# Kernel optimization log

Measured on AMD Instinct MI355X. Metric: run time of the kernel, lower is better.

Reference implementation:

```python
import jax, jax.numpy as jnp
import numpy as np

S, L, E = 64, 256, 768          # sentences, tokens per sentence, BERT hidden
N, P = 4096, 32768              # events, event pairs
C, H, D = 256, 4, 64            # CGE channels, heads, head dim (C = H*D = n_last)
M = 8                           # max event span length
MLP_H = 1024
ITERS = 3                       # max_iteration + 1
RATE = 0.5
BETA_INTRA, BETA_INTER = 0.5, 0.5


def setup_inputs():
    key = jax.random.key(0)
    ks = jax.random.split(key, 16)
    nrm = lambda k, shape, sc: jax.random.normal(k, shape, dtype=jnp.float32) * sc
    event_start = jax.random.randint(ks[2], (N,), 0, L - M)
    span = jax.random.randint(ks[3], (N,), 1, M + 1)
    return {
        "sent_emb": nrm(ks[0], (S, L, E), 1.0),
        "proj_in_W": nrm(ks[7], (E, C), E ** -0.5),
        "proj_in_b": jnp.zeros((C,), jnp.float32),
        "proj_W": nrm(ks[8], (C, C), C ** -0.5),
        "proj_b": jnp.zeros((C,), jnp.float32),
        "att_src_intra": nrm(ks[9], (H, D), D ** -0.5),
        "att_dst_intra": nrm(ks[10], (H, D), D ** -0.5),
        "att_src_inter": nrm(ks[11], (H, D), D ** -0.5),
        "att_dst_inter": nrm(ks[12], (H, D), D ** -0.5),
        "mlp_W1": nrm(ks[13], (C + 2 * E, MLP_H), (C + 2 * E) ** -0.5),
        "mlp_b1": jnp.zeros((MLP_H,), jnp.float32),
        "mlp_W2": nrm(ks[14], (MLP_H, 3), MLP_H ** -0.5),
        "mlp_b2": jnp.zeros((3,), jnp.float32),
        "event_sent": jax.random.randint(ks[1], (N,), 0, S),
        "event_start": event_start,
        "event_end": event_start + span,
        "pair_idx": jax.random.randint(ks[4], (P, 2), 0, N),
        "rel_type": jax.random.randint(ks[5], (P,), 0, 2),
        "target": jax.random.randint(ks[6], (P,), 0, 3),
    }


def _attend(h, src, dst, emask, att_src, att_dst):
    # h: [N,H,D]. Masked graph attention, softmax over incoming edges per dst.
    a = jax.nn.leaky_relu((h[src] * att_src).sum(-1) + (h[dst] * att_dst).sum(-1), 0.2)  # [En,H]
    a = jnp.where(emask[:, None], a, -1e9)
    amax = jnp.maximum(jax.ops.segment_max(a, dst, num_segments=N), -1e9)  # [N,H]
    ex = jnp.exp(a - amax[dst]) * emask[:, None].astype(a.dtype)
    denom = jax.ops.segment_sum(ex, dst, num_segments=N)
    alpha = ex / (denom[dst] + 1e-9)
    out = jax.ops.segment_sum(alpha[:, :, None] * h[src], dst, num_segments=N)  # [N,H,D]
    return out.reshape(N, H * D)


def _forward(sent_emb, proj_in_W, proj_in_b, proj_W, proj_b,
             att_src_intra, att_dst_intra, att_src_inter, att_dst_inter,
             mlp_W1, mlp_b1, mlp_W2, mlp_b2,
             event_sent, event_start, event_end, pair_idx, rel_type, target):
    # extract_event: mean of sentence token embeddings over each event span
    pos = event_start[:, None] + jnp.arange(M)                      # [N,M]
    vmask = (pos < event_end[:, None]).astype(sent_emb.dtype)       # [N,M]
    tok = sent_emb[event_sent[:, None], jnp.clip(pos, 0, L - 1)]    # [N,M,E]
    e_emb = (tok * vmask[..., None]).sum(1) / (event_end - event_start).astype(sent_emb.dtype)[:, None]

    p0, p1 = pair_idx[:, 0], pair_idx[:, 1]
    pair_emb = jnp.concatenate([e_emb[p0], e_emb[p1]], axis=-1)     # [P,2E]
    x = e_emb @ proj_in_W + proj_in_b                               # [N,C]

    self_idx = jnp.arange(N)
    ones_n = jnp.ones((N,), bool)
    src_all = jnp.concatenate([p0, p1])
    dst_all = jnp.concatenate([p1, p0])
    intra2 = jnp.concatenate([rel_type == 0, rel_type == 0])

    loss = jnp.float32(0.0)
    pred = None
    for it in range(ITERS):
        diff = x[p0] - x[p1]                                        # [P,C]
        pre = jnp.concatenate([pair_emb, diff], axis=-1)            # [P,2E+C]
        pred = jax.nn.relu(pre @ mlp_W1 + mlp_b1) @ mlp_W2 + mlp_b2  # [P,3]
        logp = jax.nn.log_softmax(pred, axis=-1)
        loss = loss + (1.0 / (it + 1)) * (-jnp.take_along_axis(logp, target[:, None], axis=1).mean())

        # data-dependent edge construction (masked, fixed-size edge lists)
        psoft = jax.nn.softmax(pred, axis=-1)
        conf = psoft.max(1) > RATE
        parg = psoft.argmax(1)
        m_all = jnp.concatenate([conf & (parg == 1), conf & (parg == 2)])

        h = (x @ proj_W + proj_b).reshape(N, H, D)
        # intra edges + always-on self loops
        src_i = jnp.concatenate([src_all, self_idx])
        dst_i = jnp.concatenate([dst_all, self_idx])
        m_i = jnp.concatenate([m_all & intra2, ones_n])
        out_intra = _attend(h, src_i, dst_i, m_i, att_src_intra, att_dst_intra)
        out_inter = _attend(h, src_all, dst_all, m_all & (~intra2), att_src_inter, att_dst_inter)
        x = BETA_INTRA * out_intra + BETA_INTER * out_inter
    return loss, pred


def reference(sent_emb, proj_in_W, proj_in_b, proj_W, proj_b,
              att_src_intra, att_dst_intra, att_src_inter, att_dst_inter,
              mlp_W1, mlp_b1, mlp_W2, mlp_b2,
              event_sent, event_start, event_end, pair_idx, rel_type, target):
    return _forward(sent_emb, proj_in_W, proj_in_b, proj_W, proj_b,
                    att_src_intra, att_dst_intra, att_src_inter, att_dst_inter,
                    mlp_W1, mlp_b1, mlp_W2, mlp_b2,
                    event_sent, event_start, event_end, pair_idx, rel_type, target)
```

## Files before the change

### kernel.cpp

```cpp
#include <hip/hip_runtime.h>
#include <cstddef>
#include <cstdint>

#define NEV   4096
#define NPAIR 32768
#define NEDGE (2*NPAIR)
#define EDIM  768
#define CDIM  256
#define MLPH  1024
#define LLEN  256

typedef unsigned short u16;
typedef __attribute__((ext_vector_type(8))) short bhalf8;
typedef __attribute__((ext_vector_type(4))) float f32x4;

#define GLOAD_LDS(g, l) __builtin_amdgcn_global_load_lds( \
    (const __attribute__((address_space(1))) unsigned int*)(g), \
    (__attribute__((address_space(3))) unsigned int*)(l), 16, 0, 0)

__device__ inline u16 f2bf(float f) {
  union { float f; unsigned u; } v; v.f = f;
  unsigned r = v.u + 0x7fffu + ((v.u >> 16) & 1u);
  return (u16)(r >> 16);
}
__device__ inline float bf2f(u16 h) {
  union { unsigned u; float f; } v; v.u = ((unsigned)h) << 16; return v.f;
}

__global__ void k_zero(int* __restrict__ deg, float* __restrict__ out) {
  int i = blockIdx.x * 256 + threadIdx.x;
  if (i < NEV) deg[i] = 0;
  if (i == 0) out[0] = 0.f;
}

__global__ void k_embed(const float* __restrict__ sent, const int* __restrict__ es,
                        const int* __restrict__ st, const int* __restrict__ en,
                        u16* __restrict__ Ahat) {
  int node = blockIdx.x;
  int s = es[node];
  int a = st[node];
  int span = en[node] - a;
  float fspan = (float)span;
  const float* base = sent + ((size_t)s * LLEN + a) * EDIM;
  for (int d = threadIdx.x; d < EDIM; d += 256) {
    float acc = 0.f;
    for (int m = 0; m < span; ++m) acc += base[(size_t)m * EDIM + d];
    float e = acc / fspan;
    u16 hi = f2bf(e);
    float lo = e - bf2f(hi);
    size_t b = (size_t)node * (3 * EDIM);
    Ahat[b + d] = hi;
    Ahat[b + EDIM + d] = hi;
    Ahat[b + 2 * EDIM + d] = f2bf(lo);
  }
}

__global__ void k_count(const int* __restrict__ pair, int* __restrict__ deg) {
  int e = blockIdx.x * 256 + threadIdx.x;
  if (e >= NEDGE) return;
  int p = (e < NPAIR) ? e : e - NPAIR;
  int dst = (e < NPAIR) ? pair[2 * p + 1] : pair[2 * p];
  atomicAdd(&deg[dst], 1);
}

__global__ void k_scan(const int* __restrict__ deg, int* __restrict__ rowp,
                       int* __restrict__ cursor) {
  __shared__ int part[256];
  int t = threadIdx.x;
  int base = t * 16;
  int sum = 0;
  for (int i = 0; i < 16; ++i) sum += deg[base + i];
  part[t] = sum;
  __syncthreads();
  for (int off = 1; off < 256; off <<= 1) {
    int v = (t >= off) ? part[t - off] : 0;
    __syncthreads();
    part[t] += v;
    __syncthreads();
  }
  int run = (t == 0) ? 0 : part[t - 1];
  for (int i = 0; i < 16; ++i) {
    rowp[base + i] = run;
    cursor[base + i] = 0;
    run += deg[base + i];
  }
  if (t == 255) rowp[NEV] = run;
}

__global__ void k_scatter(const int* __restrict__ pair, const int* __restrict__ rowp,
                          int* __restrict__ cursor, int* __restrict__ e_src,
                          int* __restrict__ e_id) {
  int e = blockIdx.x * 256 + threadIdx.x;
  if (e >= NEDGE) return;
  int p   = (e < NPAIR) ? e : e - NPAIR;
  int src = (e < NPAIR) ? pair[2 * p]     : pair[2 * p + 1];
  int dst = (e < NPAIR) ? pair[2 * p + 1] : pair[2 * p];
  int pos = rowp[dst] + atomicAdd(&cursor[dst], 1);
  e_src[pos] = src;
  e_id[pos]  = e;
}

__global__ __launch_bounds__(256) void cvt_w(const float* __restrict__ W1,
                                             const float* __restrict__ piW,
                                             const float* __restrict__ projW,
                                             u16* __restrict__ BT, int which)
{
  __shared__ float tile[32][33];
  int K = which ? CDIM : EDIM;
  int ld = K * 3;
  int bk = blockIdx.y * 32;
  int bc = blockIdx.x * 32;
  int tx = threadIdx.x & 31, ty = threadIdx.x >> 5;
#pragma unroll
  for (int rr = 0; rr < 4; ++rr) {
    int k = bk + ty + rr * 8;
    int c = bc + tx;
    float v;
    if (which == 0) {
      v = (c < 1024) ? W1[(size_t)k * MLPH + c]
        : (c < 2048) ? W1[(size_t)(EDIM + k) * MLPH + (c - 1024)]
        : piW[(size_t)k * CDIM + (c - 2048)];
    } else {
      v = (c < 1024) ? W1[(size_t)(2 * EDIM + k) * MLPH + c]
        : projW[(size_t)k * CDIM + (c - 1024)];
    }
    tile[ty + rr * 8][tx] = v;
  }
  __syncthreads();
#pragma unroll
  for (int rr = 0; rr < 4; ++rr) {
    int c = bc + ty + rr * 8;
    int k = bk + tx;
    float v = tile[tx][ty + rr * 8];
    u16 hi = f2bf(v);
    float lo = v - bf2f(hi);
    size_t b = (size_t)c * ld;
    BT[b + k] = hi;
    BT[b + K + k] = f2bf(lo);
    BT[b + 2 * K + k] = hi;
  }
}

__global__ __launch_bounds__(256) void mgemm(
    const u16* __restrict__ A, const u16* __restrict__ BT, int Kp, int mode,
    float* __restrict__ G1, float* __restrict__ G2, u16* __restrict__ Xhat,
    const float* __restrict__ pib, const float* __restrict__ b1,
    const float* __restrict__ pb, float* __restrict__ U, float* __restrict__ V,
    float* __restrict__ h)
{
  __shared__ u16 As[64 * 64];
  __shared__ u16 Bs[128 * 64];
  int tid = threadIdx.x;
  int wave = tid >> 6, lane = tid & 63;
  int bm = blockIdx.y * 64, bn = blockIdx.x * 128;
  int wm = (wave >> 1) * 32, wn = (wave & 1) * 64;

  int srow = tid >> 3;
  int scol = (tid & 7) << 3;
  const u16* Ag = A + (size_t)(bm + srow) * Kp + scol;
  const u16* Bg = BT + (size_t)(bn + srow) * Kp + scol;
  u16* Asd = &As[tid * 8];
  u16* Bsd = &Bs[tid * 8];

  f32x4 acc[2][4];
#pragma unroll
  for (int i = 0; i < 2; ++i)
#pragma unroll
    for (int j = 0; j < 4; ++j) {
      f32x4 z = {0.f, 0.f, 0.f, 0.f};
      acc[i][j] = z;
    }

  int fr = lane & 15;
  int fq = lane >> 4;

  for (int k0 = 0; k0 < Kp; k0 += 64) {
#pragma unroll
    for (int c = 0; c < 2; ++c)
      GLOAD_LDS(Ag + (size_t)(c * 32) * Kp, Asd + c * 2048);
#pragma unroll
    for (int c = 0; c < 4; ++c)
      GLOAD_LDS(Bg + (size_t)(c * 32) * Kp, Bsd + c * 2048);
    __syncthreads();
#pragma unroll
    for (int kk = 0; kk < 2; ++kk) {
      bhalf8 af[2], bf[4];
#pragma unroll
      for (int i = 0; i < 2; ++i)
        af[i] = *(const bhalf8*)&As[(wm + i * 16 + fr) * 64 + kk * 32 + fq * 8];
#pragma unroll
      for (int j = 0; j < 4; ++j)
        bf[j] = *(const bhalf8*)&Bs[(wn + j * 16 + fr) * 64 + kk * 32 + fq * 8];
#pragma unroll
      for (int i = 0; i < 2; ++i)
#pragma unroll
        for (int j = 0; j < 4; ++j)
          acc[i][j] = __builtin_amdgcn_mfma_f32_16x16x32_bf16(af[i], bf[j], acc[i][j], 0, 0, 0);
    }
    __syncthreads();
    Ag += 64;
    Bg += 64;
  }

#pragma unroll
  for (int i = 0; i < 2; ++i) {
    int mrow = bm + wm + i * 16 + fq * 4;
#pragma unroll
    for (int g = 0; g < 4; ++g) {
      int m = mrow + g;
#pragma unroll
      for (int j = 0; j < 4; ++j) {
        int c = bn + wn + j * 16 + fr;
        float vv = acc[i][j][g];
        if (mode == 0) {
          if (c < 1024) {
            G1[(size_t)m * MLPH + c] = vv;
          } else if (c < 2048) {
            G2[(size_t)m * MLPH + (c - 1024)] = vv;
          } else {
            int cc = c - 2048;
            float xv = vv + pib[cc];
            u16 hi = f2bf(xv);
            float lo = xv - bf2f(hi);
            size_t b = (size_t)m * (3 * CDIM);
            Xhat[b + cc] = hi;
            Xhat[b + CDIM + cc] = hi;
            Xhat[b + 2 * CDIM + cc] = f2bf(lo);
          }
        } else {
          if (c < 1024) {
            size_t idx = (size_t)m * MLPH + c;
            U[idx] = G1[idx] + vv + b1[c];
            V[idx] = G2[idx] - vv;
          } else {
            int cc = c - 1024;
            h[(size_t)m * CDIM + cc] = vv + pb[cc];
          }
        }
      }
    }
  }
}

__global__ void k_s(const float* __restrict__ h,
                    const float* __restrict__ asi, const float* __restrict__ adi,
                    const float* __restrict__ asj, const float* __restrict__ adj,
                    float* __restrict__ sv) {
  int node = blockIdx.x * 4 + (threadIdx.x >> 6);
  int lane = threadIdx.x & 63;
  int head = lane >> 4;
  int d0 = (lane & 15) << 2;
  float4 hv = *(const float4*)(h + (size_t)node * CDIM + head * 64 + d0);
  float4 w1 = *(const float4*)(asi + head * 64 + d0);
  float4 w2 = *(const float4*)(adi + head * 64 + d0);
  float4 w3 = *(const float4*)(asj + head * 64 + d0);
  float4 w4 = *(const float4*)(adj + head * 64 + d0);
  float p1 = hv.x * w1.x + hv.y * w1.y + hv.z * w1.z + hv.w * w1.w;
  float p2 = hv.x * w2.x + hv.y * w2.y + hv.z * w2.z + hv.w * w2.w;
  float p3 = hv.x * w3.x + hv.y * w3.y + hv.z * w3.z + hv.w * w3.w;
  float p4 = hv.x * w4.x + hv.y * w4.y + hv.z * w4.z + hv.w * w4.w;
#pragma unroll
  for (int m = 1; m < 16; m <<= 1) {
    p1 += __shfl_xor(p1, m);
    p2 += __shfl_xor(p2, m);
    p3 += __shfl_xor(p3, m);
    p4 += __shfl_xor(p4, m);
  }
  if ((lane & 15) == 0) {
    sv[0 * NEV * 4 + node * 4 + head] = p1;
    sv[1 * NEV * 4 + node * 4 + head] = p2;
    sv[2 * NEV * 4 + node * 4 + head] = p3;
    sv[3 * NEV * 4 + node * 4 + head] = p4;
  }
}

__global__ __launch_bounds__(256) void k_pred(
    const float* __restrict__ U, const float* __restrict__ V,
    const int* __restrict__ pair, const float* __restrict__ W2,
    const float* __restrict__ b2, const int* __restrict__ target,
    int* __restrict__ mstate, float* __restrict__ out,
    float* __restrict__ partials, float lossCoef)
{
  __shared__ float red[4];
  int wv = threadIdx.x >> 6;
  int p = blockIdx.x * 4 + wv;
  int lane = threadIdx.x & 63;
  int i0 = pair[2 * p], i1 = pair[2 * p + 1];
  const float* u = U + (size_t)i0 * MLPH;
  const float* v = V + (size_t)i1 * MLPH;
  float a0 = 0.f, a1 = 0.f, a2 = 0.f;
  for (int kb = (lane << 2); kb < MLPH; kb += 256) {
    float4 uu = *(const float4*)(u + kb);
    float4 vv = *(const float4*)(v + kb);
    float h0 = fmaxf(uu.x + vv.x, 0.f);
    float h1 = fmaxf(uu.y + vv.y, 0.f);
    float h2 = fmaxf(uu.z + vv.z, 0.f);
    float h3 = fmaxf(uu.w + vv.w, 0.f);
    const float4* w4 = (const float4*)(W2 + 3 * kb);
    float4 wa = w4[0], wb = w4[1], wc = w4[2];
    a0 += h0 * wa.x + h1 * wa.w + h2 * wb.z + h3 * wc.y;
    a1 += h0 * wa.y + h1 * wb.x + h2 * wb.w + h3 * wc.z;
    a2 += h0 * wa.z + h1 * wb.y + h2 * wc.x + h3 * wc.w;
  }
#pragma unroll
  for (int m = 32; m >= 1; m >>= 1) {
    a0 += __shfl_down(a0, m);
    a1 += __shfl_down(a1, m);
    a2 += __shfl_down(a2, m);
  }
  if (lane == 0) {
    a0 += b2[0]; a1 += b2[1]; a2 += b2[2];
    float mx = fmaxf(a0, fmaxf(a1, a2));
    float e0 = expf(a0 - mx), e1 = expf(a1 - mx), e2 = expf(a2 - mx);
    float sum = e0 + e1 + e2;
    int arg = 0; float best = e0;
    if (e1 > best) { best = e1; arg = 1; }
    if (e2 > best) { best = e2; arg = 2; }
    bool conf = (best / sum) > 0.5f;
    mstate[p] = conf ? arg : -1;
    int t = target[p];
    float predt = (t == 0) ? a0 : ((t == 1) ? a1 : a2);
    float logp = (predt - mx) - logf(sum);
    red[wv] = -logp * lossCoef;
    float* po = out + 1 + (size_t)p * 3;
    po[0] = a0; po[1] = a1; po[2] = a2;
  }
  __syncthreads();
  if (threadIdx.x == 0) partials[blockIdx.x] = red[0] + red[1] + red[2] + red[3];
}

__global__ void k_lossred(const float* __restrict__ partials, float* __restrict__ out, int n) {
  __shared__ float sm[256];
  float s = 0.f;
  for (int i = threadIdx.x; i < n; i += 256) s += partials[i];
  sm[threadIdx.x] = s;
  __syncthreads();
  for (int off = 128; off; off >>= 1) {
    if (threadIdx.x < off) sm[threadIdx.x] += sm[threadIdx.x + off];
    __syncthreads();
  }
  if (threadIdx.x == 0) out[0] += sm[0];
}

__global__ __launch_bounds__(256) void k_attn(
    const float* __restrict__ h, const float* __restrict__ sv,
    const int* __restrict__ rowp, const int* __restrict__ e_src,
    const int* __restrict__ e_id, const int* __restrict__ mstate,
    const int* __restrict__ rel, u16* __restrict__ Xhat)
{
  int node = blockIdx.x;
  int t = threadIdx.x;
  int head = t >> 6;
  const float* s_si = sv;
  const float* s_di = sv + NEV * 4;
  const float* s_sj = sv + 2 * NEV * 4;
  const float* s_dj = sv + 3 * NEV * 4;
  float sdi = s_di[node * 4 + head];
  float sdj = s_dj[node * 4 + head];
  int beg = rowp[node], end = rowp[node + 1];
  float aself = s_si[node * 4 + head] + sdi;
  aself = aself > 0.f ? aself : 0.2f * aself;
  float mxi = aself;
  float mxj = -1e9f;
  for (int e = beg; e < end; ++e) {
    int eid = e_id[e];
    int pp = (eid < NPAIR) ? eid : eid - NPAIR;
    int st = mstate[pp];
    bool mall = (eid < NPAIR) ? (st == 1) : (st == 2);
    if (!mall) continue;
    int src = e_src[e];
    if (rel[pp] == 0) {
      float a = s_si[src * 4 + head] + sdi;
      a = a > 0.f ? a : 0.2f * a;
      mxi = fmaxf(mxi, a);
    } else {
      float a = s_sj[src * 4 + head] + sdj;
      a = a > 0.f ? a : 0.2f * a;
      mxj = fmaxf(mxj, a);
    }
  }
  float deni = 0.f, denj = 0.f, acci = 0.f, accj = 0.f;
  {
    float ex = expf(aself - mxi);
    deni += ex;
    acci += ex * h[(size_t)node * CDIM + t];
  }
  for (int e = beg; e < end; ++e) {
    int eid = e_id[e];
    int pp = (eid < NPAIR) ? eid : eid - NPAIR;
    int st = mstate[pp];
    bool mall = (eid < NPAIR) ? (st == 1) : (st == 2);
    if (!mall) continue;
    int src = e_src[e];
    float hval = h[(size_t)src * CDIM + t];
    if (rel[pp] == 0) {
      float a = s_si[src * 4 + head] + sdi;
      a = a > 0.f ? a : 0.2f * a;
      float ex = expf(a - mxi);
      deni += ex; acci += ex * hval;
    } else {
      float a = s_sj[src * 4 + head] + sdj;
      a = a > 0.f ? a : 0.2f * a;
      float ex = expf(a - mxj);
      denj += ex; accj += ex * hval;
    }
  }
  float outv = 0.5f * (acci / (deni + 1e-9f)) + 0.5f * (accj / (denj + 1e-9f));
  u16 hi = f2bf(outv);
  float lo = outv - bf2f(hi);
  size_t b = (size_t)node * (3 * CDIM);
  Xhat[b + t] = hi;
  Xhat[b + CDIM + t] = hi;
  Xhat[b + 2 * CDIM + t] = f2bf(lo);
}

extern "C" void kernel_launch(void* const* d_in, const int* in_sizes, int n_in,
                              void* d_out, int out_size, void* d_ws, size_t ws_size,
                              hipStream_t stream)
{
  const float* sent      = (const float*)d_in[0];
  const float* proj_in_W = (const float*)d_in[1];
  const float* proj_in_b = (const float*)d_in[2];
  const float* proj_W    = (const float*)d_in[3];
  const float* proj_b    = (const float*)d_in[4];
  const float* asi       = (const float*)d_in[5];
  const float* adi       = (const float*)d_in[6];
  const float* asj       = (const float*)d_in[7];
  const float* adj       = (const float*)d_in[8];
  const float* W1        = (const float*)d_in[9];
  const float* b1        = (const float*)d_in[10];
  const float* W2        = (const float*)d_in[11];
  const float* b2        = (const float*)d_in[12];
  const int*   es        = (const int*)d_in[13];
  const int*   st        = (const int*)d_in[14];
  const int*   en        = (const int*)d_in[15];
  const int*   pair      = (const int*)d_in[16];
  const int*   rel       = (const int*)d_in[17];
  const int*   target    = (const int*)d_in[18];
  float* out = (float*)d_out;

  char* w = (char*)d_ws;
  auto alloc = [&](size_t bytes) -> char* {
    char* p = w;
    w += (bytes + 255) & ~(size_t)255;
    return p;
  };
  u16*   Ahat = (u16*)alloc(sizeof(u16) * (size_t)NEV * 3 * EDIM);
  u16*   BTe  = (u16*)alloc(sizeof(u16) * (size_t)2304 * 2304);
  u16*   BTu  = (u16*)alloc(sizeof(u16) * (size_t)1280 * 768);
  u16*   Xhat = (u16*)alloc(sizeof(u16) * (size_t)NEV * 3 * CDIM);
  float* G1   = (float*)alloc(sizeof(float) * (size_t)NEV * MLPH);
  float* G2   = (float*)alloc(sizeof(float) * (size_t)NEV * MLPH);
  float* U    = (float*)alloc(sizeof(float) * (size_t)NEV * MLPH);
  float* V    = (float*)alloc(sizeof(float) * (size_t)NEV * MLPH);
  float* h    = (float*)alloc(sizeof(float) * (size_t)NEV * CDIM);
  float* sv   = (float*)alloc(sizeof(float) * (size_t)NEV * 16);
  float* lpart= (float*)alloc(sizeof(float) * (NPAIR / 4));
  int* deg    = (int*)alloc(sizeof(int) * NEV);
  int* rowp   = (int*)alloc(sizeof(int) * (NEV + 1));
  int* cursor = (int*)alloc(sizeof(int) * NEV);
  int* e_src  = (int*)alloc(sizeof(int) * NEDGE);
  int* e_id   = (int*)alloc(sizeof(int) * NEDGE);
  int* mstate = (int*)alloc(sizeof(int) * NPAIR);

  k_zero<<<(NEV + 255) / 256, 256, 0, stream>>>(deg, out);
  k_embed<<<NEV, 256, 0, stream>>>(sent, es, st, en, Ahat);
  k_count<<<NEDGE / 256, 256, 0, stream>>>(pair, deg);
  k_scan<<<1, 256, 0, stream>>>(deg, rowp, cursor);
  k_scatter<<<NEDGE / 256, 256, 0, stream>>>(pair, rowp, cursor, e_src, e_id);

  cvt_w<<<dim3(2304 / 32, 768 / 32), 256, 0, stream>>>(W1, proj_in_W, proj_W, BTe, 0);
  cvt_w<<<dim3(1280 / 32, 256 / 32), 256, 0, stream>>>(W1, proj_in_W, proj_W, BTu, 1);

  mgemm<<<dim3(2304 / 128, NEV / 64), 256, 0, stream>>>(
      Ahat, BTe, 3 * EDIM, 0, G1, G2, Xhat, proj_in_b,
      nullptr, nullptr, nullptr, nullptr, nullptr);

  for (int it = 0; it < 3; ++it) {
    mgemm<<<dim3(1280 / 128, NEV / 64), 256, 0, stream>>>(
        Xhat, BTu, 3 * CDIM, 1, G1, G2, nullptr, nullptr,
        b1, proj_b, U, V, h);
    k_s<<<NEV / 4, 256, 0, stream>>>(h, asi, adi, asj, adj, sv);
    float coef = 1.0f / ((float)(it + 1) * (float)NPAIR);
    k_pred<<<NPAIR / 4, 256, 0, stream>>>(U, V, pair, W2, b2, target, mstate, out, lpart, coef);
    k_lossred<<<1, 256, 0, stream>>>(lpart, out, NPAIR / 4);
    k_attn<<<NEV, 256, 0, stream>>>(h, sv, rowp, e_src, e_id, mstate, rel, Xhat);
  }
  (void)in_sizes; (void)n_in; (void)out_size; (void)ws_size;
}
```

Before: 587.4 us.

## Group pair prediction by first event and shrink GEMM tiles with swizzled blocks

Builds a CSR index of pairs keyed by their first event so the pair-prediction kernel runs one block per event, stages that event's U row in shared memory once and loops over its pairs. This removes repeated global reads of U rows across pairs. Separately, the GEMM tile changes from 64x128 to 64x64 and a block-index swizzle is added, giving more workgroups and better L2 locality at the cost of more B reloads. The per-event grouping adds setup kernels and leaves load imbalance across events with uneven pair counts.

```diff
diff --git a/kernel.cpp b/kernel.cpp
--- a/kernel.cpp
+++ b/kernel.cpp
@@ -27,9 +27,10 @@
   union { unsigned u; float f; } v; v.u = ((unsigned)h) << 16; return v.f;
 }
 
-__global__ void k_zero(int* __restrict__ deg, float* __restrict__ out) {
+__global__ void k_zero(int* __restrict__ deg, int* __restrict__ pdeg,
+                       float* __restrict__ out) {
   int i = blockIdx.x * 256 + threadIdx.x;
-  if (i < NEV) deg[i] = 0;
+  if (i < NEV) { deg[i] = 0; pdeg[i] = 0; }
   if (i == 0) out[0] = 0.f;
 }
 
@@ -100,6 +101,20 @@
   e_id[pos]  = e;
 }
 
+__global__ void k_pcount(const int* __restrict__ pair, int* __restrict__ pdeg) {
+  int p = blockIdx.x * 256 + threadIdx.x;
+  if (p >= NPAIR) return;
+  atomicAdd(&pdeg[pair[2 * p]], 1);
+}
+
+__global__ void k_pscatter(const int* __restrict__ pair, const int* __restrict__ prow,
+                           int* __restrict__ pcur, int* __restrict__ pidx) {
+  int p = blockIdx.x * 256 + threadIdx.x;
+  if (p >= NPAIR) return;
+  int pos = prow[pair[2 * p]] + atomicAdd(&pcur[pair[2 * p]], 1);
+  pidx[pos] = p;
+}
+
 __global__ __launch_bounds__(256) void cvt_w(const float* __restrict__ W1,
                                              const float* __restrict__ piW,
                                              const float* __restrict__ projW,
@@ -149,11 +164,17 @@
     float* __restrict__ h)
 {
   __shared__ u16 As[64 * 64];
-  __shared__ u16 Bs[128 * 64];
+  __shared__ u16 Bs[64 * 64];
   int tid = threadIdx.x;
   int wave = tid >> 6, lane = tid & 63;
-  int bm = blockIdx.y * 64, bn = blockIdx.x * 128;
-  int wm = (wave >> 1) * 32, wn = (wave & 1) * 64;
+
+  int gx = gridDim.x;
+  int nwg = gx * gridDim.y;
+  int orig = blockIdx.y * gx + blockIdx.x;
+  int swz = (orig & 7) * (nwg >> 3) + (orig >> 3);
+  int bm = (swz / gx) * 64, bn = (swz % gx) * 64;
+
+  int wm = (wave >> 1) * 32, wn = (wave & 1) * 32;
 
   int srow = tid >> 3;
   int scol = (tid & 7) << 3;
@@ -162,11 +183,11 @@
   u16* Asd = &As[tid * 8];
   u16* Bsd = &Bs[tid * 8];
 
-  f32x4 acc[2][4];
+  f32x4 acc[2][2];
 #pragma unroll
   for (int i = 0; i < 2; ++i)
 #pragma unroll
-    for (int j = 0; j < 4; ++j) {
+    for (int j = 0; j < 2; ++j) {
       f32x4 z = {0.f, 0.f, 0.f, 0.f};
       acc[i][j] = z;
     }
@@ -176,25 +197,24 @@
 
   for (int k0 = 0; k0 < Kp; k0 += 64) {
 #pragma unroll
-    for (int c = 0; c < 2; ++c)
+    for (int c = 0; c < 2; ++c) {
       GLOAD_LDS(Ag + (size_t)(c * 32) * Kp, Asd + c * 2048);
-#pragma unroll
-    for (int c = 0; c < 4; ++c)
       GLOAD_LDS(Bg + (size_t)(c * 32) * Kp, Bsd + c * 2048);
+    }
     __syncthreads();
 #pragma unroll
     for (int kk = 0; kk < 2; ++kk) {
-      bhalf8 af[2], bf[4];
+      bhalf8 af[2], bf[2];
 #pragma unroll
       for (int i = 0; i < 2; ++i)
         af[i] = *(const bhalf8*)&As[(wm + i * 16 + fr) * 64 + kk * 32 + fq * 8];
 #pragma unroll
-      for (int j = 0; j < 4; ++j)
+      for (int j = 0; j < 2; ++j)
         bf[j] = *(const bhalf8*)&Bs[(wn + j * 16 + fr) * 64 + kk * 32 + fq * 8];
 #pragma unroll
       for (int i = 0; i < 2; ++i)
 #pragma unroll
-        for (int j = 0; j < 4; ++j)
+        for (int j = 0; j < 2; ++j)
           acc[i][j] = __builtin_amdgcn_mfma_f32_16x16x32_bf16(af[i], bf[j], acc[i][j], 0, 0, 0);
     }
     __syncthreads();
@@ -209,7 +229,7 @@
     for (int g = 0; g < 4; ++g) {
       int m = mrow + g;
 #pragma unroll
-      for (int j = 0; j < 4; ++j) {
+      for (int j = 0; j < 2; ++j) {
         int c = bn + wn + j * 16 + fr;
         float vv = acc[i][j][g];
         if (mode == 0) {
@@ -274,59 +294,70 @@
   }
 }
 
-__global__ __launch_bounds__(256) void k_pred(
+__global__ __launch_bounds__(256) void k_pred_g(
     const float* __restrict__ U, const float* __restrict__ V,
-    const int* __restrict__ pair, const float* __restrict__ W2,
+    const int* __restrict__ pair, const int* __restrict__ prow,
+    const int* __restrict__ pidx, const float* __restrict__ W2,
     const float* __restrict__ b2, const int* __restrict__ target,
     int* __restrict__ mstate, float* __restrict__ out,
     float* __restrict__ partials, float lossCoef)
 {
+  __shared__ float ush[MLPH];
   __shared__ float red[4];
-  int wv = threadIdx.x >> 6;
-  int p = blockIdx.x * 4 + wv;
-  int lane = threadIdx.x & 63;
-  int i0 = pair[2 * p], i1 = pair[2 * p + 1];
-  const float* u = U + (size_t)i0 * MLPH;
-  const float* v = V + (size_t)i1 * MLPH;
-  float a0 = 0.f, a1 = 0.f, a2 = 0.f;
-  for (int kb = (lane << 2); kb < MLPH; kb += 256) {
-    float4 uu = *(const float4*)(u + kb);
-    float4 vv = *(const float4*)(v + kb);
-    float h0 = fmaxf(uu.x + vv.x, 0.f);
-    float h1 = fmaxf(uu.y + vv.y, 0.f);
-    float h2 = fmaxf(uu.z + vv.z, 0.f);
-    float h3 = fmaxf(uu.w + vv.w, 0.f);
-    const float4* w4 = (const float4*)(W2 + 3 * kb);
-    float4 wa = w4[0], wb = w4[1], wc = w4[2];
-    a0 += h0 * wa.x + h1 * wa.w + h2 * wb.z + h3 * wc.y;
-    a1 += h0 * wa.y + h1 * wb.x + h2 * wb.w + h3 * wc.z;
-    a2 += h0 * wa.z + h1 * wb.y + h2 * wc.x + h3 * wc.w;
-  }
-#pragma unroll
-  for (int m = 32; m >= 1; m >>= 1) {
-    a0 += __shfl_down(a0, m);
-    a1 += __shfl_down(a1, m);
-    a2 += __shfl_down(a2, m);
-  }
-  if (lane == 0) {
-    a0 += b2[0]; a1 += b2[1]; a2 += b2[2];
-    float mx = fmaxf(a0, fmaxf(a1, a2));
-    float e0 = expf(a0 - mx), e1 = expf(a1 - mx), e2 = expf(a2 - mx);
-    float sum = e0 + e1 + e2;
-    int arg = 0; float best = e0;
-    if (e1 > best) { best = e1; arg = 1; }
-    if (e2 > best) { best = e2; arg = 2; }
-    bool conf = (best / sum) > 0.5f;
-    mstate[p] = conf ? arg : -1;
-    int t = target[p];
-    float predt = (t == 0) ? a0 : ((t == 1) ? a1 : a2);
-    float logp = (predt - mx) - logf(sum);
-    red[wv] = -logp * lossCoef;
-    float* po = out + 1 + (size_t)p * 3;
-    po[0] = a0; po[1] = a1; po[2] = a2;
-  }
+  int n = blockIdx.x;
+  int tid = threadIdx.x;
+  const float* u = U + (size_t)n * MLPH;
+#pragma unroll
+  for (int i = 0; i < 4; ++i) ush[tid + i * 256] = u[tid + i * 256];
   __syncthreads();
-  if (threadIdx.x == 0) partials[blockIdx.x] = red[0] + red[1] + red[2] + red[3];
+  int wv = tid >> 6, lane = tid & 63;
+  int beg = prow[n], end = prow[n + 1];
+  float lsum = 0.f;
+  for (int ip = beg + wv; ip < end; ip += 4) {
+    int p = pidx[ip];
+    int i1 = pair[2 * p + 1];
+    const float* v = V + (size_t)i1 * MLPH;
+    float a0 = 0.f, a1 = 0.f, a2 = 0.f;
+    for (int kb = (lane << 2); kb < MLPH; kb += 256) {
+      float4 uu = *(const float4*)(&ush[kb]);
+      float4 vv = *(const float4*)(v + kb);
+      float h0 = fmaxf(uu.x + vv.x, 0.f);
+      float h1 = fmaxf(uu.y + vv.y, 0.f);
+      float h2 = fmaxf(uu.z + vv.z, 0.f);
+      float h3 = fmaxf(uu.w + vv.w, 0.f);
+      const float4* w4 = (const float4*)(W2 + 3 * kb);
+      float4 wa = w4[0], wb = w4[1], wc = w4[2];
+      a0 += h0 * wa.x + h1 * wa.w + h2 * wb.z + h3 * wc.y;
+      a1 += h0 * wa.y + h1 * wb.x + h2 * wb.w + h3 * wc.z;
+      a2 += h0 * wa.z + h1 * wb.y + h2 * wc.x + h3 * wc.w;
+    }
+#pragma unroll
+    for (int m = 32; m >= 1; m >>= 1) {
+      a0 += __shfl_down(a0, m);
+      a1 += __shfl_down(a1, m);
+      a2 += __shfl_down(a2, m);
+    }
+    if (lane == 0) {
+      a0 += b2[0]; a1 += b2[1]; a2 += b2[2];
+      float mx = fmaxf(a0, fmaxf(a1, a2));
+      float e0 = expf(a0 - mx), e1 = expf(a1 - mx), e2 = expf(a2 - mx);
+      float sum = e0 + e1 + e2;
+      int arg = 0; float best = e0;
+      if (e1 > best) { best = e1; arg = 1; }
+      if (e2 > best) { best = e2; arg = 2; }
+      bool conf = (best / sum) > 0.5f;
+      mstate[p] = conf ? arg : -1;
+      int t = target[p];
+      float predt = (t == 0) ? a0 : ((t == 1) ? a1 : a2);
+      float logp = (predt - mx) - logf(sum);
+      lsum += -logp * lossCoef;
+      float* po = out + 1 + (size_t)p * 3;
+      po[0] = a0; po[1] = a1; po[2] = a2;
+    }
+  }
+  if (lane == 0) red[wv] = lsum;
+  __syncthreads();
+  if (tid == 0) partials[n] = red[0] + red[1] + red[2] + red[3];
 }
 
 __global__ void k_lossred(const float* __restrict__ partials, float* __restrict__ out, int n) {
@@ -455,35 +486,43 @@
   float* V    = (float*)alloc(sizeof(float) * (size_t)NEV * MLPH);
   float* h    = (float*)alloc(sizeof(float) * (size_t)NEV * CDIM);
   float* sv   = (float*)alloc(sizeof(float) * (size_t)NEV * 16);
-  float* lpart= (float*)alloc(sizeof(float) * (NPAIR / 4));
+  float* lpart= (float*)alloc(sizeof(float) * NEV);
   int* deg    = (int*)alloc(sizeof(int) * NEV);
   int* rowp   = (int*)alloc(sizeof(int) * (NEV + 1));
   int* cursor = (int*)alloc(sizeof(int) * NEV);
   int* e_src  = (int*)alloc(sizeof(int) * NEDGE);
   int* e_id   = (int*)alloc(sizeof(int) * NEDGE);
+  int* pdeg   = (int*)alloc(sizeof(int) * NEV);
+  int* prow   = (int*)alloc(sizeof(int) * (NEV + 1));
+  int* pcur   = (int*)alloc(sizeof(int) * NEV);
+  int* pidx   = (int*)alloc(sizeof(int) * NPAIR);
   int* mstate = (int*)alloc(sizeof(int) * NPAIR);
 
-  k_zero<<<(NEV + 255) / 256, 256, 0, stream>>>(deg, out);
+  k_zero<<<(NEV + 255) / 256, 256, 0, stream>>>(deg, pdeg, out);
   k_embed<<<NEV, 256, 0, stream>>>(sent, es, st, en, Ahat);
   k_count<<<NEDGE / 256, 256, 0, stream>>>(pair, deg);
   k_scan<<<1, 256, 0, stream>>>(deg, rowp, cursor);
   k_scatter<<<NEDGE / 256, 256, 0, stream>>>(pair, rowp, cursor, e_src, e_id);
+  k_pcount<<<NPAIR / 256, 256, 0, stream>>>(pair, pdeg);
+  k_scan<<<1, 256, 0, stream>>>(pdeg, prow, pcur);
+  k_pscatter<<<NPAIR / 256, 256, 0, stream>>>(pair, prow, pcur, pidx);
 
   cvt_w<<<dim3(2304 / 32, 768 / 32), 256, 0, stream>>>(W1, proj_in_W, proj_W, BTe, 0);
   cvt_w<<<dim3(1280 / 32, 256 / 32), 256, 0, stream>>>(W1, proj_in_W, proj_W, BTu, 1);
 
-  mgemm<<<dim3(2304 / 128, NEV / 64), 256, 0, stream>>>(
+  mgemm<<<dim3(2304 / 64, NEV / 64), 256, 0, stream>>>(
       Ahat, BTe, 3 * EDIM, 0, G1, G2, Xhat, proj_in_b,
       nullptr, nullptr, nullptr, nullptr, nullptr);
 
   for (int it = 0; it < 3; ++it) {
-    mgemm<<<dim3(1280 / 128, NEV / 64), 256, 0, stream>>>(
+    mgemm<<<dim3(1280 / 64, NEV / 64), 256, 0, stream>>>(
         Xhat, BTu, 3 * CDIM, 1, G1, G2, nullptr, nullptr,
         b1, proj_b, U, V, h);
     k_s<<<NEV / 4, 256, 0, stream>>>(h, asi, adi, asj, adj, sv);
     float coef = 1.0f / ((float)(it + 1) * (float)NPAIR);
-    k_pred<<<NPAIR / 4, 256, 0, stream>>>(U, V, pair, W2, b2, target, mstate, out, lpart, coef);
-    k_lossred<<<1, 256, 0, stream>>>(lpart, out, NPAIR / 4);
+    k_pred_g<<<NEV, 256, 0, stream>>>(U, V, pair, prow, pidx, W2, b2, target,
+                                      mstate, out, lpart, coef);
+    k_lossred<<<1, 256, 0, stream>>>(lpart, out, NEV);
     k_attn<<<NEV, 256, 0, stream>>>(h, sv, rowp, e_src, e_id, mstate, rel, Xhat);
   }
   (void)in_sizes; (void)n_in; (void)out_size; (void)ws_size;
```

Measured after the change: 574.6 us. -2.2%, faster.
